# Kernel optimization log

Measured on AMD Instinct MI355X. Metric: run time of the kernel, lower is better.

The kernel has to match this reference:

```python
import jax, jax.numpy as jnp
import numpy as np

B, S, D, H = 2, 2048, 1024, 16
HD = D // H

def setup_inputs() -> dict:
    key = jax.random.key(0)
    ks = jax.random.split(key, 11)
    s = 1.0 / np.sqrt(D)
    return {
        "query": jax.random.normal(ks[0], (B, S, D), jnp.float32),
        "key": jax.random.normal(ks[1], (B, S, D), jnp.float32),
        "value": jax.random.normal(ks[2], (B, S, D), jnp.float32),
        "Wq": jax.random.normal(ks[3], (D, D), jnp.float32) * s,
        "bq": jax.random.normal(ks[4], (D,), jnp.float32) * s,
        "Wk": jax.random.normal(ks[5], (D, D), jnp.float32) * s,
        "bk": jax.random.normal(ks[6], (D,), jnp.float32) * s,
        "Wv": jax.random.normal(ks[7], (D, D), jnp.float32) * s,
        "bv": jax.random.normal(ks[8], (D,), jnp.float32) * s,
        "Wo": jax.random.normal(ks[9], (D, D), jnp.float32) * s,
        "bo": jax.random.normal(ks[10], (D,), jnp.float32) * s,
        "test": 0,
    }

def _heads(x, W, b):
    # [B,S,D] @ [D,D] -> [B,S,D] -> [B,H,S,HD]
    y = x @ W + b
    return y.reshape(B, -1, H, HD).transpose(0, 2, 1, 3)

def reference(query, key, value, Wq, bq, Wk, bk, Wv, bv, Wo, bo, test):
    q = _heads(query, Wq, bq)
    k = _heads(key, Wk, bk)
    v = _heads(value, Wv, bv)
    scale = 1.0 / np.sqrt(HD).astype(np.float32)
    scores = jnp.einsum('bhqd,bhkd->bhqk', q, k) * scale  # [B,H,S,S]
    if test:
        return scores
    prob = jax.nn.softmax(scores, axis=-1)
    out = jnp.einsum('bhqk,bhkd->bhqd', prob, v)
    out = out.transpose(0, 2, 1, 3).reshape(B, -1, D)
    return out @ Wo + bo
```

## Files before the change

### kernel.cpp

```cpp
#include <hip/hip_runtime.h>

constexpr int Bn  = 2;
constexpr int Sn  = 2048;
constexpr int Dn  = 1024;
constexpr int Hn  = 16;
constexpr int HDn = 64;
constexpr int Mn  = Bn * Sn;

typedef _Float16 half8 __attribute__((ext_vector_type(8)));
typedef _Float16 half4 __attribute__((ext_vector_type(4)));
typedef float    f32x4 __attribute__((ext_vector_type(4)));

__device__ __forceinline__ void cp16(const _Float16* g, _Float16* l) {
  __builtin_amdgcn_global_load_lds(
      (__attribute__((address_space(1))) void*)g,
      (__attribute__((address_space(3))) void*)l, 16, 0, 0);
}

__global__ __launch_bounds__(256) void convert_x(
    const float* __restrict__ q, const float* __restrict__ k,
    const float* __restrict__ v, _Float16* __restrict__ Xh) {
  const int z = blockIdx.y;
  const float* src = (z == 0) ? q : (z == 1) ? k : v;
  _Float16* dst = Xh + (size_t)z * (Mn * Dn);
  int i = blockIdx.x * 256 + threadIdx.x;
  float4 v4 = ((const float4*)src)[i];
  half4 h;
  h.x = (_Float16)v4.x; h.y = (_Float16)v4.y;
  h.z = (_Float16)v4.z; h.w = (_Float16)v4.w;
  *(half4*)(dst + (size_t)i * 4) = h;
}

__global__ __launch_bounds__(256) void transpose_w(
    const float* __restrict__ Wq, const float* __restrict__ Wk,
    const float* __restrict__ Wv, const float* __restrict__ Wo,
    _Float16* __restrict__ WT) {
  const int z = blockIdx.z;
  const float* W = (z == 0) ? Wq : (z == 1) ? Wk : (z == 2) ? Wv : Wo;
  _Float16* T = WT + (size_t)z * Dn * Dn;
  __shared__ float tile[64][65];
  const int k0 = blockIdx.y * 64, n0 = blockIdx.x * 64;
  const int tid = threadIdx.x;
#pragma unroll
  for (int i = 0; i < 4; i++) {
    int s = tid + i * 256;
    int r = s >> 4, c4 = s & 15;
    float4 w4 = *(const float4*)(W + (size_t)(k0 + r) * Dn + n0 + c4 * 4);
    tile[r][c4 * 4 + 0] = w4.x; tile[r][c4 * 4 + 1] = w4.y;
    tile[r][c4 * 4 + 2] = w4.z; tile[r][c4 * 4 + 3] = w4.w;
  }
  __syncthreads();
#pragma unroll
  for (int i = 0; i < 2; i++) {
    int s = tid + i * 256;
    int n = s >> 3, r8 = (s & 7) * 8;
    half8 h;
#pragma unroll
    for (int j = 0; j < 8; j++) h[j] = (_Float16)tile[r8 + j][n];
    *(half8*)(T + (size_t)(n0 + n) * Dn + k0 + r8) = h;
  }
}

__global__ __launch_bounds__(256) void proj_kernel(
    const _Float16* __restrict__ Xh, const _Float16* __restrict__ WT,
    const float* __restrict__ bq, const float* __restrict__ bk,
    const float* __restrict__ bv,
    _Float16* __restrict__ Qh, _Float16* __restrict__ Kh,
    _Float16* __restrict__ VT) {
  const int z = blockIdx.z;
  const _Float16* A  = Xh + (size_t)z * Mn * Dn;
  const _Float16* Bm = WT + (size_t)z * Dn * Dn;
  const float* bias = (z == 0) ? bq : (z == 1) ? bk : bv;

  __shared__ __align__(16) _Float16 As[128 * 32];
  __shared__ __align__(16) _Float16 Bs[128 * 32];

  const int tid  = threadIdx.x;
  const int lane = tid & 63;
  const int w    = tid >> 6;
  const int wm   = (w >> 1) * 64;
  const int wn   = (w & 1) * 64;
  const int m0   = blockIdx.y * 128;
  const int n0   = blockIdx.x * 128;
  const int qd   = lane >> 4;
  const int lm   = lane & 15;

  f32x4 acc[4][4];
#pragma unroll
  for (int i = 0; i < 4; i++)
#pragma unroll
    for (int j = 0; j < 4; j++) acc[i][j] = {0.f, 0.f, 0.f, 0.f};

  for (int k0 = 0; k0 < Dn; k0 += 32) {
#pragma unroll
    for (int p = 0; p < 2; p++) {
      int s = tid + p * 256;
      int row = s >> 2, c = s & 3;
      cp16(A + (size_t)(m0 + row) * Dn + k0 + c * 8, As + s * 8);
    }
#pragma unroll
    for (int p = 0; p < 2; p++) {
      int s = tid + p * 256;
      int row = s >> 2, c = s & 3;
      cp16(Bm + (size_t)(n0 + row) * Dn + k0 + c * 8, Bs + s * 8);
    }
    __syncthreads();
    half8 a[4], bb[4];
#pragma unroll
    for (int mi = 0; mi < 4; mi++)
      a[mi] = *(const half8*)(As + (wm + mi * 16 + lm) * 32 + qd * 8);
#pragma unroll
    for (int ni = 0; ni < 4; ni++)
      bb[ni] = *(const half8*)(Bs + (wn + ni * 16 + lm) * 32 + qd * 8);
    if (z < 2) {
#pragma unroll
      for (int mi = 0; mi < 4; mi++)
#pragma unroll
        for (int ni = 0; ni < 4; ni++)
          acc[mi][ni] = __builtin_amdgcn_mfma_f32_16x16x32_f16(bb[ni], a[mi], acc[mi][ni], 0, 0, 0);
    } else {
#pragma unroll
      for (int mi = 0; mi < 4; mi++)
#pragma unroll
        for (int ni = 0; ni < 4; ni++)
          acc[mi][ni] = __builtin_amdgcn_mfma_f32_16x16x32_f16(a[mi], bb[ni], acc[mi][ni], 0, 0, 0);
    }
    __syncthreads();
  }

  if (z < 2) {
    _Float16* out = (z == 0) ? Qh : Kh;
    const float scl = (z == 0) ? 0.125f * 1.44269504089f : 1.0f;
#pragma unroll
    for (int mi = 0; mi < 4; mi++) {
      int m = m0 + wm + mi * 16 + lm;
      int b_ = m >> 11, s_ = m & (Sn - 1);
#pragma unroll
      for (int ni = 0; ni < 4; ni++) {
        int nb = n0 + wn + ni * 16 + qd * 4;
        float4 b4 = *(const float4*)(bias + nb);
        int h = nb >> 6, hd = nb & 63;
        half4 h4;
        h4[0] = (_Float16)((acc[mi][ni][0] + b4.x) * scl);
        h4[1] = (_Float16)((acc[mi][ni][1] + b4.y) * scl);
        h4[2] = (_Float16)((acc[mi][ni][2] + b4.z) * scl);
        h4[3] = (_Float16)((acc[mi][ni][3] + b4.w) * scl);
        *(half4*)(out + (((size_t)(b_ * Hn + h)) * Sn + s_) * HDn + hd) = h4;
      }
    }
  } else {
#pragma unroll
    for (int ni = 0; ni < 4; ni++) {
      int n = n0 + wn + ni * 16 + lm;
      float b_f = bias[n];
      int h = n >> 6, hd = n & 63;
#pragma unroll
      for (int mi = 0; mi < 4; mi++) {
        int mb = m0 + wm + mi * 16 + qd * 4;
        int b_ = mb >> 11, s_ = mb & (Sn - 1);
        half4 h4;
#pragma unroll
        for (int r = 0; r < 4; r++) h4[r] = (_Float16)(acc[mi][ni][r] + b_f);
        *(half4*)(VT + (((size_t)(b_ * Hn + h)) * HDn + hd) * Sn + s_) = h4;
      }
    }
  }
}

__global__ __launch_bounds__(256, 3) void attn_kernel(
    const _Float16* __restrict__ Qh, const _Float16* __restrict__ Kh,
    const _Float16* __restrict__ VT, _Float16* __restrict__ attn_out) {
  constexpr int PV_LD = 72;
  __shared__ __align__(16) _Float16 Ksb[2][128 * 64];
  __shared__ __align__(16) _Float16 Ps[4 * 32 * PV_LD];

  const int n    = blockIdx.x;
  const int slot = n >> 3;
  const int bh   = (n & 7) * 4 + (slot >> 4);
  const int q0   = (slot & 15) * 128;
  const size_t base = (size_t)bh * Sn * HDn;

  const int tid  = threadIdx.x;
  const int lane = tid & 63;
  const int w    = tid >> 6;
  const int qd   = lane >> 4;
  const int lm   = lane & 15;

  const _Float16* qptr = Qh + base + (size_t)(q0 + w * 32 + lm) * HDn + qd * 8;
  half8 qa[2][2];
#pragma unroll
  for (int nj = 0; nj < 2; nj++)
#pragma unroll
    for (int ks = 0; ks < 2; ks++)
      qa[nj][ks] = *(const half8*)(qptr + nj * 16 * HDn + ks * 32);

  half8 vones;
#pragma unroll
  for (int j = 0; j < 8; j++) vones[j] = (lm == 0) ? (_Float16)1.0f : (_Float16)0.0f;

  f32x4 oacc[2][4];
#pragma unroll
  for (int i = 0; i < 2; i++)
#pragma unroll
    for (int j = 0; j < 4; j++) oacc[i][j] = {0.f, 0.f, 0.f, 0.f};
  f32x4 oaccl[2] = {{0.f, 0.f, 0.f, 0.f}, {0.f, 0.f, 0.f, 0.f}};

  _Float16* Psw = Ps + w * (32 * PV_LD);
  const f32x4 sinit = {-10.f, -10.f, -10.f, -10.f};

  const int st_r = tid >> 3;
  const int st_u = (tid & 7) ^ (st_r & 7);
  const _Float16* kbase = Kh + base;

#define STAGE_K(KT, DST)                                                     \
  {                                                                          \
    const _Float16* src_ = kbase + (size_t)(KT) * 128 * HDn;                 \
    _Float16* dst_ = (DST);                                                  \
    _Pragma("unroll")                                                        \
    for (int p = 0; p < 4; p++)                                              \
      cp16(src_ + (size_t)(st_r + p * 32) * HDn + st_u * 8,                  \
           dst_ + (tid + p * 256) * 8);                                      \
  }

  STAGE_K(0, Ksb[0])
  __syncthreads();

  int cur = 0;
  for (int kt = 0; kt < Sn / 128; kt++) {
    const int kb = kt * 128;
    if (kt + 1 < Sn / 128) STAGE_K(kt + 1, Ksb[cur ^ 1])

#pragma unroll
    for (int c = 0; c < 2; c++) {
      f32x4 sacc[4][2];
#pragma unroll
      for (int n4 = 0; n4 < 4; n4++)
#pragma unroll
        for (int nj = 0; nj < 2; nj++) sacc[n4][nj] = sinit;
#pragma unroll
      for (int n4 = 0; n4 < 4; n4++) {
        int ni = 4 * c + n4;
#pragma unroll
        for (int ks = 0; ks < 2; ks++) {
          int up = (4 * ks + qd) ^ (lm & 7);
          half8 ka = *(const half8*)(Ksb[cur] + (ni * 16 + lm) * HDn + up * 8);
#pragma unroll
          for (int nj = 0; nj < 2; nj++)
            sacc[n4][nj] = __builtin_amdgcn_mfma_f32_16x16x32_f16(ka, qa[nj][ks], sacc[n4][nj], 0, 0, 0);
        }
      }

      half8 vb[4][2];
#pragma unroll
      for (int oi = 0; oi < 4; oi++)
#pragma unroll
        for (int k2 = 0; k2 < 2; k2++)
          vb[oi][k2] = *(const half8*)(VT + base + (size_t)(oi * 16 + lm) * Sn
                                       + kb + c * 64 + k2 * 32 + qd * 8);

#pragma unroll
      for (int nj = 0; nj < 2; nj++)
#pragma unroll
        for (int n4 = 0; n4 < 4; n4++) {
          float p0 = __builtin_amdgcn_exp2f(sacc[n4][nj][0]);
          float p1 = __builtin_amdgcn_exp2f(sacc[n4][nj][1]);
          float p2 = __builtin_amdgcn_exp2f(sacc[n4][nj][2]);
          float p3 = __builtin_amdgcn_exp2f(sacc[n4][nj][3]);
          auto lo = __builtin_amdgcn_cvt_pkrtz(p0, p1);
          auto hi = __builtin_amdgcn_cvt_pkrtz(p2, p3);
          half4 h4;
          h4[0] = (_Float16)lo[0]; h4[1] = (_Float16)lo[1];
          h4[2] = (_Float16)hi[0]; h4[3] = (_Float16)hi[1];
          *(half4*)(Psw + (nj * 16 + lm) * PV_LD + n4 * 16 + qd * 4) = h4;
        }

#pragma unroll
      for (int k2 = 0; k2 < 2; k2++) {
        half8 pa[2];
#pragma unroll
        for (int mi = 0; mi < 2; mi++)
          pa[mi] = *(const half8*)(Psw + (mi * 16 + lm) * PV_LD + k2 * 32 + qd * 8);
#pragma unroll
        for (int oi = 0; oi < 4; oi++)
#pragma unroll
          for (int mi = 0; mi < 2; mi++)
            oacc[mi][oi] = __builtin_amdgcn_mfma_f32_16x16x32_f16(vb[oi][k2], pa[mi], oacc[mi][oi], 0, 0, 0);
#pragma unroll
        for (int mi = 0; mi < 2; mi++)
          oaccl[mi] = __builtin_amdgcn_mfma_f32_16x16x32_f16(vones, pa[mi], oaccl[mi], 0, 0, 0);
      }
    }

    __syncthreads();
    cur ^= 1;
  }
#undef STAGE_K

  const int b_ = bh >> 4, h_ = bh & 15;
#pragma unroll
  for (int mi = 0; mi < 2; mi++) {
    float lr = __shfl(oaccl[mi][0], lm, 64);
    float inv = 1.0f / lr;
    int qrow = q0 + w * 32 + mi * 16 + lm;
    size_t rowbase = ((size_t)(b_ * Sn + qrow)) * Dn + h_ * 64;
#pragma unroll
    for (int oi = 0; oi < 4; oi++) {
      half4 h4;
#pragma unroll
      for (int r = 0; r < 4; r++) h4[r] = (_Float16)(oacc[mi][oi][r] * inv);
      *(half4*)(attn_out + rowbase + oi * 16 + qd * 4) = h4;
    }
  }
}

__global__ __launch_bounds__(256) void outproj_kernel(
    const _Float16* __restrict__ Aattn, const _Float16* __restrict__ WoT,
    const float* __restrict__ bo, float* __restrict__ out) {
  __shared__ __align__(16) _Float16 As[128 * 32];
  __shared__ __align__(16) _Float16 Bs[128 * 32];

  const int tid  = threadIdx.x;
  const int lane = tid & 63;
  const int w    = tid >> 6;
  const int wm   = (w >> 1) * 64;
  const int wn   = (w & 1) * 64;
  const int m0   = blockIdx.y * 128;
  const int n0   = blockIdx.x * 128;
  const int qd   = lane >> 4;
  const int lm   = lane & 15;

  f32x4 acc[4][4];
#pragma unroll
  for (int i = 0; i < 4; i++)
#pragma unroll
    for (int j = 0; j < 4; j++) acc[i][j] = {0.f, 0.f, 0.f, 0.f};

  for (int k0 = 0; k0 < Dn; k0 += 32) {
#pragma unroll
    for (int p = 0; p < 2; p++) {
      int s = tid + p * 256;
      int row = s >> 2, c = s & 3;
      cp16(Aattn + (size_t)(m0 + row) * Dn + k0 + c * 8, As + s * 8);
    }
#pragma unroll
    for (int p = 0; p < 2; p++) {
      int s = tid + p * 256;
      int row = s >> 2, c = s & 3;
      cp16(WoT + (size_t)(n0 + row) * Dn + k0 + c * 8, Bs + s * 8);
    }
    __syncthreads();
    half8 a[4], bb[4];
#pragma unroll
    for (int mi = 0; mi < 4; mi++)
      a[mi] = *(const half8*)(As + (wm + mi * 16 + lm) * 32 + qd * 8);
#pragma unroll
    for (int ni = 0; ni < 4; ni++)
      bb[ni] = *(const half8*)(Bs + (wn + ni * 16 + lm) * 32 + qd * 8);
#pragma unroll
    for (int mi = 0; mi < 4; mi++)
#pragma unroll
      for (int ni = 0; ni < 4; ni++)
        acc[mi][ni] = __builtin_amdgcn_mfma_f32_16x16x32_f16(bb[ni], a[mi], acc[mi][ni], 0, 0, 0);
    __syncthreads();
  }
#pragma unroll
  for (int mi = 0; mi < 4; mi++) {
    int m = m0 + wm + mi * 16 + lm;
#pragma unroll
    for (int ni = 0; ni < 4; ni++) {
      int nb = n0 + wn + ni * 16 + qd * 4;
      float4 b4 = *(const float4*)(bo + nb);
      float4 o4;
      o4.x = acc[mi][ni][0] + b4.x;
      o4.y = acc[mi][ni][1] + b4.y;
      o4.z = acc[mi][ni][2] + b4.z;
      o4.w = acc[mi][ni][3] + b4.w;
      *(float4*)(out + (size_t)m * Dn + nb) = o4;
    }
  }
}

extern "C" void kernel_launch(void* const* d_in, const int* in_sizes, int n_in,
                              void* d_out, int out_size, void* d_ws, size_t ws_size,
                              hipStream_t stream) {
  const float* query = (const float*)d_in[0];
  const float* key_  = (const float*)d_in[1];
  const float* value = (const float*)d_in[2];
  const float* Wq = (const float*)d_in[3];
  const float* bq = (const float*)d_in[4];
  const float* Wk = (const float*)d_in[5];
  const float* bk = (const float*)d_in[6];
  const float* Wv = (const float*)d_in[7];
  const float* bv = (const float*)d_in[8];
  const float* Wo = (const float*)d_in[9];
  const float* bo = (const float*)d_in[10];

  _Float16* Xh = (_Float16*)d_ws;
  _Float16* WT = Xh + (size_t)3 * Mn * Dn;
  _Float16* Qh = WT + (size_t)4 * Dn * Dn;
  _Float16* Kh = Qh + (size_t)Mn * Dn;
  _Float16* VT = Kh + (size_t)Mn * Dn;
  _Float16* attnb = Xh;
  float* out = (float*)d_out;

  dim3 blk(256);
  convert_x<<<dim3((Mn * Dn) / (4 * 256), 3), blk, 0, stream>>>(query, key_, value, Xh);
  transpose_w<<<dim3(16, 16, 4), blk, 0, stream>>>(Wq, Wk, Wv, Wo, WT);
  proj_kernel<<<dim3(Dn / 128, Mn / 128, 3), blk, 0, stream>>>(
      Xh, WT, bq, bk, bv, Qh, Kh, VT);
  attn_kernel<<<dim3(512), blk, 0, stream>>>(Qh, Kh, VT, attnb);
  outproj_kernel<<<dim3(Dn / 128, Mn / 128), blk, 0, stream>>>(
      attnb, WT + (size_t)3 * Dn * Dn, bo, out);
}
```

Before: 274.6 us.

## Split attention over two KV halves, merge prep kernels, shrink outproj tile

The attention kernel now splits each query tile's key range into two halves, which doubles the grid to 1024 blocks. Each block writes an unnormalized fp32 partial output and row sum, and a new reduce kernel adds the halves, normalizes and writes fp16. This works because the softmax uses a fixed offset rather than a running max, so the partials can simply be summed. The input conversion and weight transpose kernels are merged into one launch, and the output projection uses 64-row tiles to double its block count. The cost is extra fp32 partial traffic to global memory and one more kernel launch.

```diff
diff --git a/kernel.cpp b/kernel.cpp
--- a/kernel.cpp
+++ b/kernel.cpp
@@ -17,47 +17,49 @@
       (__attribute__((address_space(3))) void*)l, 16, 0, 0);
 }
 
-__global__ __launch_bounds__(256) void convert_x(
+__global__ __launch_bounds__(256) void prep_kernel(
     const float* __restrict__ q, const float* __restrict__ k,
-    const float* __restrict__ v, _Float16* __restrict__ Xh) {
-  const int z = blockIdx.y;
-  const float* src = (z == 0) ? q : (z == 1) ? k : v;
-  _Float16* dst = Xh + (size_t)z * (Mn * Dn);
-  int i = blockIdx.x * 256 + threadIdx.x;
-  float4 v4 = ((const float4*)src)[i];
-  half4 h;
-  h.x = (_Float16)v4.x; h.y = (_Float16)v4.y;
-  h.z = (_Float16)v4.z; h.w = (_Float16)v4.w;
-  *(half4*)(dst + (size_t)i * 4) = h;
-}
-
-__global__ __launch_bounds__(256) void transpose_w(
+    const float* __restrict__ v,
     const float* __restrict__ Wq, const float* __restrict__ Wk,
     const float* __restrict__ Wv, const float* __restrict__ Wo,
-    _Float16* __restrict__ WT) {
-  const int z = blockIdx.z;
-  const float* W = (z == 0) ? Wq : (z == 1) ? Wk : (z == 2) ? Wv : Wo;
-  _Float16* T = WT + (size_t)z * Dn * Dn;
+    _Float16* __restrict__ Xh, _Float16* __restrict__ WT) {
   __shared__ float tile[64][65];
-  const int k0 = blockIdx.y * 64, n0 = blockIdx.x * 64;
+  const int n = blockIdx.x;
   const int tid = threadIdx.x;
-#pragma unroll
-  for (int i = 0; i < 4; i++) {
-    int s = tid + i * 256;
-    int r = s >> 4, c4 = s & 15;
-    float4 w4 = *(const float4*)(W + (size_t)(k0 + r) * Dn + n0 + c4 * 4);
-    tile[r][c4 * 4 + 0] = w4.x; tile[r][c4 * 4 + 1] = w4.y;
-    tile[r][c4 * 4 + 2] = w4.z; tile[r][c4 * 4 + 3] = w4.w;
-  }
-  __syncthreads();
-#pragma unroll
-  for (int i = 0; i < 2; i++) {
-    int s = tid + i * 256;
-    int n = s >> 3, r8 = (s & 7) * 8;
-    half8 h;
-#pragma unroll
-    for (int j = 0; j < 8; j++) h[j] = (_Float16)tile[r8 + j][n];
-    *(half8*)(T + (size_t)(n0 + n) * Dn + k0 + r8) = h;
+  if (n < 12288) {
+    const int z = n >> 12;
+    const float* src = (z == 0) ? q : (z == 1) ? k : v;
+    _Float16* dst = Xh + (size_t)z * (Mn * Dn);
+    int i = (n & 4095) * 256 + tid;
+    float4 v4 = ((const float4*)src)[i];
+    half4 h;
+    h.x = (_Float16)v4.x; h.y = (_Float16)v4.y;
+    h.z = (_Float16)v4.z; h.w = (_Float16)v4.w;
+    *(half4*)(dst + (size_t)i * 4) = h;
+  } else {
+    const int m = n - 12288;
+    const int z = m >> 8, rem = m & 255;
+    const float* W = (z == 0) ? Wq : (z == 1) ? Wk : (z == 2) ? Wv : Wo;
+    _Float16* T = WT + (size_t)z * Dn * Dn;
+    const int k0 = (rem >> 4) * 64, n0 = (rem & 15) * 64;
+#pragma unroll
+    for (int i = 0; i < 4; i++) {
+      int s = tid + i * 256;
+      int r = s >> 4, c4 = s & 15;
+      float4 w4 = *(const float4*)(W + (size_t)(k0 + r) * Dn + n0 + c4 * 4);
+      tile[r][c4 * 4 + 0] = w4.x; tile[r][c4 * 4 + 1] = w4.y;
+      tile[r][c4 * 4 + 2] = w4.z; tile[r][c4 * 4 + 3] = w4.w;
+    }
+    __syncthreads();
+#pragma unroll
+    for (int i = 0; i < 2; i++) {
+      int s = tid + i * 256;
+      int nn = s >> 3, r8 = (s & 7) * 8;
+      half8 h;
+#pragma unroll
+      for (int j = 0; j < 8; j++) h[j] = (_Float16)tile[r8 + j][nn];
+      *(half8*)(T + (size_t)(n0 + nn) * Dn + k0 + r8) = h;
+    }
   }
 }
 
@@ -169,15 +171,17 @@
 
 __global__ __launch_bounds__(256, 3) void attn_kernel(
     const _Float16* __restrict__ Qh, const _Float16* __restrict__ Kh,
-    const _Float16* __restrict__ VT, _Float16* __restrict__ attn_out) {
+    const _Float16* __restrict__ VT, float* __restrict__ Op,
+    float* __restrict__ Lp) {
   constexpr int PV_LD = 72;
   __shared__ __align__(16) _Float16 Ksb[2][128 * 64];
   __shared__ __align__(16) _Float16 Ps[4 * 32 * PV_LD];
 
   const int n    = blockIdx.x;
   const int slot = n >> 3;
-  const int bh   = (n & 7) * 4 + (slot >> 4);
-  const int q0   = (slot & 15) * 128;
+  const int bh   = (n & 7) * 4 + (slot >> 5);
+  const int q0   = ((slot & 31) >> 1) * 128;
+  const int kvh  = slot & 1;
   const size_t base = (size_t)bh * Sn * HDn;
 
   const int tid  = threadIdx.x;
@@ -222,13 +226,14 @@
            dst_ + (tid + p * 256) * 8);                                      \
   }
 
-  STAGE_K(0, Ksb[0])
+  const int kt0 = kvh * 8, kt1 = kt0 + 8;
+  STAGE_K(kt0, Ksb[0])
   __syncthreads();
 
   int cur = 0;
-  for (int kt = 0; kt < Sn / 128; kt++) {
+  for (int kt = kt0; kt < kt1; kt++) {
     const int kb = kt * 128;
-    if (kt + 1 < Sn / 128) STAGE_K(kt + 1, Ksb[cur ^ 1])
+    if (kt + 1 < kt1) STAGE_K(kt + 1, Ksb[cur ^ 1])
 
 #pragma unroll
     for (int c = 0; c < 2; c++) {
@@ -296,51 +301,68 @@
   }
 #undef STAGE_K
 
-  const int b_ = bh >> 4, h_ = bh & 15;
+  float* opb = Op + (((size_t)kvh * 32 + bh) * Sn) * HDn;
 #pragma unroll
   for (int mi = 0; mi < 2; mi++) {
-    float lr = __shfl(oaccl[mi][0], lm, 64);
-    float inv = 1.0f / lr;
     int qrow = q0 + w * 32 + mi * 16 + lm;
-    size_t rowbase = ((size_t)(b_ * Sn + qrow)) * Dn + h_ * 64;
 #pragma unroll
     for (int oi = 0; oi < 4; oi++) {
-      half4 h4;
-#pragma unroll
-      for (int r = 0; r < 4; r++) h4[r] = (_Float16)(oacc[mi][oi][r] * inv);
-      *(half4*)(attn_out + rowbase + oi * 16 + qd * 4) = h4;
-    }
-  }
+      f32x4 o4 = oacc[mi][oi];
+      *(f32x4*)(opb + (size_t)qrow * HDn + oi * 16 + qd * 4) = o4;
+    }
+    if (qd == 0)
+      Lp[((size_t)kvh * 32 + bh) * Sn + qrow] = oaccl[mi][0];
+  }
+}
+
+__global__ __launch_bounds__(256) void attn_reduce(
+    const float* __restrict__ Op, const float* __restrict__ Lp,
+    _Float16* __restrict__ attnb) {
+  const int idx = blockIdx.x * 256 + threadIdx.x;
+  const int t   = idx >> 8;
+  const int r   = idx & 255;
+  const int h   = r >> 4;
+  const int hd4 = (r & 15) * 4;
+  const int b_  = t >> 11, s_ = t & (Sn - 1);
+  const int bh  = b_ * Hn + h;
+  const size_t o0 = ((size_t)bh * Sn + s_) * HDn + hd4;
+  const size_t o1 = ((size_t)(32 + bh) * Sn + s_) * HDn + hd4;
+  f32x4 a = *(const f32x4*)(Op + o0);
+  f32x4 b = *(const f32x4*)(Op + o1);
+  float l = Lp[(size_t)bh * Sn + s_] + Lp[(size_t)(32 + bh) * Sn + s_];
+  float inv = 1.0f / l;
+  half4 h4;
+#pragma unroll
+  for (int j = 0; j < 4; j++) h4[j] = (_Float16)((a[j] + b[j]) * inv);
+  *(half4*)(attnb + (size_t)t * Dn + h * 64 + hd4) = h4;
 }
 
 __global__ __launch_bounds__(256) void outproj_kernel(
     const _Float16* __restrict__ Aattn, const _Float16* __restrict__ WoT,
     const float* __restrict__ bo, float* __restrict__ out) {
-  __shared__ __align__(16) _Float16 As[128 * 32];
+  __shared__ __align__(16) _Float16 As[64 * 32];
   __shared__ __align__(16) _Float16 Bs[128 * 32];
 
   const int tid  = threadIdx.x;
   const int lane = tid & 63;
   const int w    = tid >> 6;
-  const int wm   = (w >> 1) * 64;
+  const int wm   = (w >> 1) * 32;
   const int wn   = (w & 1) * 64;
-  const int m0   = blockIdx.y * 128;
+  const int m0   = blockIdx.y * 64;
   const int n0   = blockIdx.x * 128;
   const int qd   = lane >> 4;
   const int lm   = lane & 15;
 
-  f32x4 acc[4][4];
-#pragma unroll
-  for (int i = 0; i < 4; i++)
+  f32x4 acc[2][4];
+#pragma unroll
+  for (int i = 0; i < 2; i++)
 #pragma unroll
     for (int j = 0; j < 4; j++) acc[i][j] = {0.f, 0.f, 0.f, 0.f};
 
   for (int k0 = 0; k0 < Dn; k0 += 32) {
-#pragma unroll
-    for (int p = 0; p < 2; p++) {
-      int s = tid + p * 256;
-      int row = s >> 2, c = s & 3;
-      cp16(Aattn + (size_t)(m0 + row) * Dn + k0 + c * 8, As + s * 8);
+    {
+      int row = tid >> 2, c = tid & 3;
+      cp16(Aattn + (size_t)(m0 + row) * Dn + k0 + c * 8, As + tid * 8);
     }
 #pragma unroll
     for (int p = 0; p < 2; p++) {
@@ -349,22 +371,22 @@
       cp16(WoT + (size_t)(n0 + row) * Dn + k0 + c * 8, Bs + s * 8);
     }
     __syncthreads();
-    half8 a[4], bb[4];
-#pragma unroll
-    for (int mi = 0; mi < 4; mi++)
+    half8 a[2], bb[4];
+#pragma unroll
+    for (int mi = 0; mi < 2; mi++)
       a[mi] = *(const half8*)(As + (wm + mi * 16 + lm) * 32 + qd * 8);
 #pragma unroll
     for (int ni = 0; ni < 4; ni++)
       bb[ni] = *(const half8*)(Bs + (wn + ni * 16 + lm) * 32 + qd * 8);
 #pragma unroll
-    for (int mi = 0; mi < 4; mi++)
+    for (int mi = 0; mi < 2; mi++)
 #pragma unroll
       for (int ni = 0; ni < 4; ni++)
         acc[mi][ni] = __builtin_amdgcn_mfma_f32_16x16x32_f16(bb[ni], a[mi], acc[mi][ni], 0, 0, 0);
     __syncthreads();
   }
 #pragma unroll
-  for (int mi = 0; mi < 4; mi++) {
+  for (int mi = 0; mi < 2; mi++) {
     int m = m0 + wm + mi * 16 + lm;
 #pragma unroll
     for (int ni = 0; ni < 4; ni++) {
@@ -400,15 +422,18 @@
   _Float16* Qh = WT + (size_t)4 * Dn * Dn;
   _Float16* Kh = Qh + (size_t)Mn * Dn;
   _Float16* VT = Kh + (size_t)Mn * Dn;
+  float*    Op = (float*)(VT + (size_t)Mn * Dn);
+  float*    Lp = Op + (size_t)2 * 32 * Sn * HDn;
   _Float16* attnb = Xh;
   float* out = (float*)d_out;
 
   dim3 blk(256);
-  convert_x<<<dim3((Mn * Dn) / (4 * 256), 3), blk, 0, stream>>>(query, key_, value, Xh);
-  transpose_w<<<dim3(16, 16, 4), blk, 0, stream>>>(Wq, Wk, Wv, Wo, WT);
+  prep_kernel<<<dim3(12288 + 1024), blk, 0, stream>>>(
+      query, key_, value, Wq, Wk, Wv, Wo, Xh, WT);
   proj_kernel<<<dim3(Dn / 128, Mn / 128, 3), blk, 0, stream>>>(
       Xh, WT, bq, bk, bv, Qh, Kh, VT);
-  attn_kernel<<<dim3(512), blk, 0, stream>>>(Qh, Kh, VT, attnb);
-  outproj_kernel<<<dim3(Dn / 128, Mn / 128), blk, 0, stream>>>(
+  attn_kernel<<<dim3(1024), blk, 0, stream>>>(Qh, Kh, VT, Op, Lp);
+  attn_reduce<<<dim3((Mn * Dn / 4) / 256), blk, 0, stream>>>(Op, Lp, attnb);
+  outproj_kernel<<<dim3(Dn / 128, Mn / 64), blk, 0, stream>>>(
       attnb, WT + (size_t)3 * Dn * Dn, bo, out);
 }
```

After: 279.8 us. No clear change (+1.9%).

## Merge prep kernels, deepen GEMM K-tile with XOR-swizzled LDS, shrink outproj tile

Applied to the files above, without the earlier changes.

Fuses the fp32-to-fp16 input conversion and the weight transpose into one launch. The projection and output-projection GEMMs now load a 64-wide K slice per iteration, which halves the number of barrier pairs per tile, and use an XOR swizzle on the 16-byte LDS chunks to avoid bank conflicts on fragment reads. The output projection switches to 64x128 tiles so it launches twice as many blocks and fills more CUs. LDS use per block grows, which may reduce occupancy.

```diff
diff --git a/kernel.cpp b/kernel.cpp
--- a/kernel.cpp
+++ b/kernel.cpp
@@ -17,47 +17,49 @@
       (__attribute__((address_space(3))) void*)l, 16, 0, 0);
 }
 
-__global__ __launch_bounds__(256) void convert_x(
+__global__ __launch_bounds__(256) void prep_kernel(
     const float* __restrict__ q, const float* __restrict__ k,
-    const float* __restrict__ v, _Float16* __restrict__ Xh) {
-  const int z = blockIdx.y;
-  const float* src = (z == 0) ? q : (z == 1) ? k : v;
-  _Float16* dst = Xh + (size_t)z * (Mn * Dn);
-  int i = blockIdx.x * 256 + threadIdx.x;
-  float4 v4 = ((const float4*)src)[i];
-  half4 h;
-  h.x = (_Float16)v4.x; h.y = (_Float16)v4.y;
-  h.z = (_Float16)v4.z; h.w = (_Float16)v4.w;
-  *(half4*)(dst + (size_t)i * 4) = h;
-}
-
-__global__ __launch_bounds__(256) void transpose_w(
+    const float* __restrict__ v,
     const float* __restrict__ Wq, const float* __restrict__ Wk,
     const float* __restrict__ Wv, const float* __restrict__ Wo,
-    _Float16* __restrict__ WT) {
-  const int z = blockIdx.z;
-  const float* W = (z == 0) ? Wq : (z == 1) ? Wk : (z == 2) ? Wv : Wo;
-  _Float16* T = WT + (size_t)z * Dn * Dn;
+    _Float16* __restrict__ Xh, _Float16* __restrict__ WT) {
   __shared__ float tile[64][65];
-  const int k0 = blockIdx.y * 64, n0 = blockIdx.x * 64;
+  const int n = blockIdx.x;
   const int tid = threadIdx.x;
-#pragma unroll
-  for (int i = 0; i < 4; i++) {
-    int s = tid + i * 256;
-    int r = s >> 4, c4 = s & 15;
-    float4 w4 = *(const float4*)(W + (size_t)(k0 + r) * Dn + n0 + c4 * 4);
-    tile[r][c4 * 4 + 0] = w4.x; tile[r][c4 * 4 + 1] = w4.y;
-    tile[r][c4 * 4 + 2] = w4.z; tile[r][c4 * 4 + 3] = w4.w;
-  }
-  __syncthreads();
-#pragma unroll
-  for (int i = 0; i < 2; i++) {
-    int s = tid + i * 256;
-    int n = s >> 3, r8 = (s & 7) * 8;
-    half8 h;
-#pragma unroll
-    for (int j = 0; j < 8; j++) h[j] = (_Float16)tile[r8 + j][n];
-    *(half8*)(T + (size_t)(n0 + n) * Dn + k0 + r8) = h;
+  if (n < 12288) {
+    const int z = n >> 12;
+    const float* src = (z == 0) ? q : (z == 1) ? k : v;
+    _Float16* dst = Xh + (size_t)z * (Mn * Dn);
+    int i = (n & 4095) * 256 + tid;
+    float4 v4 = ((const float4*)src)[i];
+    half4 h;
+    h.x = (_Float16)v4.x; h.y = (_Float16)v4.y;
+    h.z = (_Float16)v4.z; h.w = (_Float16)v4.w;
+    *(half4*)(dst + (size_t)i * 4) = h;
+  } else {
+    const int m = n - 12288;
+    const int z = m >> 8, rem = m & 255;
+    const float* W = (z == 0) ? Wq : (z == 1) ? Wk : (z == 2) ? Wv : Wo;
+    _Float16* T = WT + (size_t)z * Dn * Dn;
+    const int k0 = (rem >> 4) * 64, n0 = (rem & 15) * 64;
+#pragma unroll
+    for (int i = 0; i < 4; i++) {
+      int s = tid + i * 256;
+      int r = s >> 4, c4 = s & 15;
+      float4 w4 = *(const float4*)(W + (size_t)(k0 + r) * Dn + n0 + c4 * 4);
+      tile[r][c4 * 4 + 0] = w4.x; tile[r][c4 * 4 + 1] = w4.y;
+      tile[r][c4 * 4 + 2] = w4.z; tile[r][c4 * 4 + 3] = w4.w;
+    }
+    __syncthreads();
+#pragma unroll
+    for (int i = 0; i < 2; i++) {
+      int s = tid + i * 256;
+      int nn = s >> 3, r8 = (s & 7) * 8;
+      half8 h;
+#pragma unroll
+      for (int j = 0; j < 8; j++) h[j] = (_Float16)tile[r8 + j][nn];
+      *(half8*)(T + (size_t)(n0 + nn) * Dn + k0 + r8) = h;
+    }
   }
 }
 
@@ -72,8 +74,8 @@
   const _Float16* Bm = WT + (size_t)z * Dn * Dn;
   const float* bias = (z == 0) ? bq : (z == 1) ? bk : bv;
 
-  __shared__ __align__(16) _Float16 As[128 * 32];
-  __shared__ __align__(16) _Float16 Bs[128 * 32];
+  __shared__ __align__(16) _Float16 As[128 * 64];
+  __shared__ __align__(16) _Float16 Bs[128 * 64];
 
   const int tid  = threadIdx.x;
   const int lane = tid & 63;
@@ -85,45 +87,46 @@
   const int qd   = lane >> 4;
   const int lm   = lane & 15;
 
+  const int st_r = tid >> 3;
+  const int st_u = (tid & 7) ^ (st_r & 7);
+
   f32x4 acc[4][4];
 #pragma unroll
   for (int i = 0; i < 4; i++)
 #pragma unroll
     for (int j = 0; j < 4; j++) acc[i][j] = {0.f, 0.f, 0.f, 0.f};
 
-  for (int k0 = 0; k0 < Dn; k0 += 32) {
-#pragma unroll
-    for (int p = 0; p < 2; p++) {
-      int s = tid + p * 256;
-      int row = s >> 2, c = s & 3;
-      cp16(A + (size_t)(m0 + row) * Dn + k0 + c * 8, As + s * 8);
-    }
-#pragma unroll
-    for (int p = 0; p < 2; p++) {
-      int s = tid + p * 256;
-      int row = s >> 2, c = s & 3;
-      cp16(Bm + (size_t)(n0 + row) * Dn + k0 + c * 8, Bs + s * 8);
-    }
-    __syncthreads();
-    half8 a[4], bb[4];
-#pragma unroll
-    for (int mi = 0; mi < 4; mi++)
-      a[mi] = *(const half8*)(As + (wm + mi * 16 + lm) * 32 + qd * 8);
-#pragma unroll
-    for (int ni = 0; ni < 4; ni++)
-      bb[ni] = *(const half8*)(Bs + (wn + ni * 16 + lm) * 32 + qd * 8);
-    if (z < 2) {
+  for (int k0 = 0; k0 < Dn; k0 += 64) {
+#pragma unroll
+    for (int p = 0; p < 4; p++) {
+      int row = st_r + p * 32;
+      cp16(A + (size_t)(m0 + row) * Dn + k0 + st_u * 8, As + (tid + p * 256) * 8);
+      cp16(Bm + (size_t)(n0 + row) * Dn + k0 + st_u * 8, Bs + (tid + p * 256) * 8);
+    }
+    __syncthreads();
+#pragma unroll
+    for (int ks = 0; ks < 2; ks++) {
+      const int up = ((ks * 4 + qd) ^ (lm & 7)) * 8;
+      half8 a[4], bb[4];
 #pragma unroll
       for (int mi = 0; mi < 4; mi++)
-#pragma unroll
-        for (int ni = 0; ni < 4; ni++)
-          acc[mi][ni] = __builtin_amdgcn_mfma_f32_16x16x32_f16(bb[ni], a[mi], acc[mi][ni], 0, 0, 0);
-    } else {
-#pragma unroll
-      for (int mi = 0; mi < 4; mi++)
-#pragma unroll
-        for (int ni = 0; ni < 4; ni++)
-          acc[mi][ni] = __builtin_amdgcn_mfma_f32_16x16x32_f16(a[mi], bb[ni], acc[mi][ni], 0, 0, 0);
+        a[mi] = *(const half8*)(As + (wm + mi * 16 + lm) * 64 + up);
+#pragma unroll
+      for (int ni = 0; ni < 4; ni++)
+        bb[ni] = *(const half8*)(Bs + (wn + ni * 16 + lm) * 64 + up);
+      if (z < 2) {
+#pragma unroll
+        for (int mi = 0; mi < 4; mi++)
+#pragma unroll
+          for (int ni = 0; ni < 4; ni++)
+            acc[mi][ni] = __builtin_amdgcn_mfma_f32_16x16x32_f16(bb[ni], a[mi], acc[mi][ni], 0, 0, 0);
+      } else {
+#pragma unroll
+        for (int mi = 0; mi < 4; mi++)
+#pragma unroll
+          for (int ni = 0; ni < 4; ni++)
+            acc[mi][ni] = __builtin_amdgcn_mfma_f32_16x16x32_f16(a[mi], bb[ni], acc[mi][ni], 0, 0, 0);
+      }
     }
     __syncthreads();
   }
@@ -316,55 +319,60 @@
 __global__ __launch_bounds__(256) void outproj_kernel(
     const _Float16* __restrict__ Aattn, const _Float16* __restrict__ WoT,
     const float* __restrict__ bo, float* __restrict__ out) {
-  __shared__ __align__(16) _Float16 As[128 * 32];
-  __shared__ __align__(16) _Float16 Bs[128 * 32];
+  __shared__ __align__(16) _Float16 As[64 * 64];
+  __shared__ __align__(16) _Float16 Bs[128 * 64];
 
   const int tid  = threadIdx.x;
   const int lane = tid & 63;
   const int w    = tid >> 6;
-  const int wm   = (w >> 1) * 64;
+  const int wm   = (w >> 1) * 32;
   const int wn   = (w & 1) * 64;
-  const int m0   = blockIdx.y * 128;
+  const int m0   = blockIdx.y * 64;
   const int n0   = blockIdx.x * 128;
   const int qd   = lane >> 4;
   const int lm   = lane & 15;
 
-  f32x4 acc[4][4];
-#pragma unroll
-  for (int i = 0; i < 4; i++)
+  const int st_r = tid >> 3;
+  const int st_u = (tid & 7) ^ (st_r & 7);
+
+  f32x4 acc[2][4];
+#pragma unroll
+  for (int i = 0; i < 2; i++)
 #pragma unroll
     for (int j = 0; j < 4; j++) acc[i][j] = {0.f, 0.f, 0.f, 0.f};
 
-  for (int k0 = 0; k0 < Dn; k0 += 32) {
+  for (int k0 = 0; k0 < Dn; k0 += 64) {
 #pragma unroll
     for (int p = 0; p < 2; p++) {
-      int s = tid + p * 256;
-      int row = s >> 2, c = s & 3;
-      cp16(Aattn + (size_t)(m0 + row) * Dn + k0 + c * 8, As + s * 8);
-    }
-#pragma unroll
-    for (int p = 0; p < 2; p++) {
-      int s = tid + p * 256;
-      int row = s >> 2, c = s & 3;
-      cp16(WoT + (size_t)(n0 + row) * Dn + k0 + c * 8, Bs + s * 8);
-    }
-    __syncthreads();
-    half8 a[4], bb[4];
-#pragma unroll
-    for (int mi = 0; mi < 4; mi++)
-      a[mi] = *(const half8*)(As + (wm + mi * 16 + lm) * 32 + qd * 8);
-#pragma unroll
-    for (int ni = 0; ni < 4; ni++)
-      bb[ni] = *(const half8*)(Bs + (wn + ni * 16 + lm) * 32 + qd * 8);
-#pragma unroll
-    for (int mi = 0; mi < 4; mi++)
+      int row = st_r + p * 32;
+      cp16(Aattn + (size_t)(m0 + row) * Dn + k0 + st_u * 8, As + (tid + p * 256) * 8);
+    }
+#pragma unroll
+    for (int p = 0; p < 4; p++) {
+      int row = st_r + p * 32;
+      cp16(WoT + (size_t)(n0 + row) * Dn + k0 + st_u * 8, Bs + (tid + p * 256) * 8);
+    }
+    __syncthreads();
+#pragma unroll
+    for (int ks = 0; ks < 2; ks++) {
+      const int up = ((ks * 4 + qd) ^ (lm & 7)) * 8;
+      half8 a[2], bb[4];
+#pragma unroll
+      for (int mi = 0; mi < 2; mi++)
+        a[mi] = *(const half8*)(As + (wm + mi * 16 + lm) * 64 + up);
 #pragma unroll
       for (int ni = 0; ni < 4; ni++)
-        acc[mi][ni] = __builtin_amdgcn_mfma_f32_16x16x32_f16(bb[ni], a[mi], acc[mi][ni], 0, 0, 0);
-    __syncthreads();
-  }
-#pragma unroll
-  for (int mi = 0; mi < 4; mi++) {
+        bb[ni] = *(const half8*)(Bs + (wn + ni * 16 + lm) * 64 + up);
+#pragma unroll
+      for (int mi = 0; mi < 2; mi++)
+#pragma unroll
+        for (int ni = 0; ni < 4; ni++)
+          acc[mi][ni] = __builtin_amdgcn_mfma_f32_16x16x32_f16(bb[ni], a[mi], acc[mi][ni], 0, 0, 0);
+    }
+    __syncthreads();
+  }
+#pragma unroll
+  for (int mi = 0; mi < 2; mi++) {
     int m = m0 + wm + mi * 16 + lm;
 #pragma unroll
     for (int ni = 0; ni < 4; ni++) {
@@ -404,11 +412,11 @@
   float* out = (float*)d_out;
 
   dim3 blk(256);
-  convert_x<<<dim3((Mn * Dn) / (4 * 256), 3), blk, 0, stream>>>(query, key_, value, Xh);
-  transpose_w<<<dim3(16, 16, 4), blk, 0, stream>>>(Wq, Wk, Wv, Wo, WT);
+  prep_kernel<<<dim3(12288 + 1024), blk, 0, stream>>>(
+      query, key_, value, Wq, Wk, Wv, Wo, Xh, WT);
   proj_kernel<<<dim3(Dn / 128, Mn / 128, 3), blk, 0, stream>>>(
       Xh, WT, bq, bk, bv, Qh, Kh, VT);
   attn_kernel<<<dim3(512), blk, 0, stream>>>(Qh, Kh, VT, attnb);
-  outproj_kernel<<<dim3(Dn / 128, Mn / 128), blk, 0, stream>>>(
+  outproj_kernel<<<dim3(Dn / 128, Mn / 64), blk, 0, stream>>>(
       attnb, WT + (size_t)3 * Dn * Dn, bo, out);
 }
```

Result: faster. 255.9 us (-6.8%).
